# Kernel optimization log

Measured on AMD Instinct MI355X. Metric: run time of the kernel, lower is better.

Reference implementation:

```python
import jax, jax.numpy as jnp
import numpy as np

N, D, H, E, K = 65536, 128, 256, 32, 2


def setup_inputs() -> dict:
    key = jax.random.key(0)
    ks = jax.random.split(key, 7)
    s_in = 1.0 / np.sqrt(D)
    s_hid = 1.0 / np.sqrt(H)
    return {
        "x": jax.random.normal(ks[0], (N, D), dtype=jnp.float32),
        "W1": jax.random.uniform(ks[1], (E, D, H), jnp.float32, -s_in, s_in),
        "b1": jax.random.uniform(ks[2], (E, H), jnp.float32, -s_in, s_in),
        "W2": jax.random.uniform(ks[3], (E, H, D), jnp.float32, -s_hid, s_hid),
        "b2": jax.random.uniform(ks[4], (E, D), jnp.float32, -s_hid, s_hid),
        "Wr": jax.random.uniform(ks[5], (D, E), jnp.float32, -s_in, s_in),
        "br": jax.random.uniform(ks[6], (E,), jnp.float32, -s_in, s_in),
    }


def reference(x, W1, b1, W2, b2, Wr, br):
    # Router (eval mode: no gate noise)
    logits = x @ Wr + br                                  # [N, E]
    scores = jax.nn.softmax(logits, axis=-1)              # [N, E]
    topk_vals, topk_inds = jax.lax.top_k(scores, K)       # [N, K]

    # dispatch_mask: zeros scattered with top-k probs (scatter_ on dim 1)
    n = x.shape[0]
    dispatch_mask = jnp.zeros_like(scores).at[
        jnp.arange(n)[:, None], topk_inds
    ].set(topk_vals)                                      # [N, E]

    # Dense all-experts compute, as in the reference torch.stack
    h = jax.nn.relu(jnp.einsum("nd,edh->neh", x, W1) + b1)   # [N, E, H]
    expert_outputs = jnp.einsum("neh,ehd->ned", h, W2) + b2  # [N, E, D]

    output = jnp.einsum("ned,ne->nd", expert_outputs, dispatch_mask)  # [N, D]

    importance = dispatch_mask.sum(axis=0)                # [E]
    imp_mean = jnp.mean(importance)
    imp_var = jnp.var(importance, ddof=1)                 # torch.var is unbiased
    load_balancing_loss = imp_var / (imp_mean ** 2 + 1e-9)
    return output, load_balancing_loss
```

## Files before the change

kernel.cpp:

```cpp
#include <hip/hip_runtime.h>
#include <hip/hip_bf16.h>
#include <cstdint>
#include <cstddef>

#define N_TOK 65536
#define DIM 128
#define HID 256
#define NE 32
#define TOPK 2

typedef __bf16 bf16x8 __attribute__((ext_vector_type(8)));
typedef float f32x4 __attribute__((ext_vector_type(4)));
typedef unsigned uint4v __attribute__((ext_vector_type(4)));

__device__ __forceinline__ unsigned short f2bf(float f) {
  unsigned u = __builtin_bit_cast(unsigned, f);
  u += 0x7fffu + ((u >> 16) & 1u);
  return (unsigned short)(u >> 16);
}
__device__ __forceinline__ float bf2f(unsigned s) {
  return __builtin_bit_cast(float, s << 16);
}
__device__ __forceinline__ uint2 split2(float f0, float f1) {
  unsigned u0 = __builtin_bit_cast(unsigned, f0);
  unsigned u1 = __builtin_bit_cast(unsigned, f1);
  unsigned hi = (u0 >> 16) | (u1 & 0xffff0000u);
  float r0 = f0 - __builtin_bit_cast(float, u0 & 0xffff0000u);
  float r1 = f1 - __builtin_bit_cast(float, u1 & 0xffff0000u);
  unsigned lo = (__builtin_bit_cast(unsigned, r0) >> 16) |
                (__builtin_bit_cast(unsigned, r1) & 0xffff0000u);
  uint2 ret; ret.x = hi; ret.y = lo;
  return ret;
}

__global__ void k_zero_out(float* __restrict__ out) {
  int t = blockIdx.x * 256 + threadIdx.x;
  float4 z = make_float4(0.f, 0.f, 0.f, 0.f);
  float4* o4 = (float4*)out;
  o4[t] = z;
  o4[t + 1048576] = z;
}

__global__ void k_weights(const float* __restrict__ W1, const float* __restrict__ W2,
                          const float* __restrict__ Wr,
                          unsigned short* __restrict__ w1t, unsigned short* __restrict__ w2t,
                          double* __restrict__ wrt64, unsigned short* __restrict__ wrb,
                          float* __restrict__ ws32, int* __restrict__ n_suspect) {
  int b = blockIdx.x;
  if (b == 512) {
    if (threadIdx.x == 0) *n_suspect = 0;
#pragma unroll
    for (int j = 0; j < 16; ++j) {
      int idx = j * 256 + threadIdx.x;
      int e = idx >> 7, d = idx & 127;
      wrt64[idx] = (double)Wr[d * NE + e];
    }
#pragma unroll
    for (int j = 0; j < 16; ++j) {
      int idx = j * 256 + threadIdx.x;
      int k = idx >> 5, e = idx & 31;
      float w = Wr[k * NE + e];
      unsigned u = __builtin_bit_cast(unsigned, w);
      unsigned short hs = (unsigned short)(u >> 16);
      float r = w - __builtin_bit_cast(float, u & 0xffff0000u);
      unsigned short ls = (unsigned short)(__builtin_bit_cast(unsigned, r) >> 16);
      int nt = e >> 4, n = e & 15, kc = k >> 5, q = (k >> 3) & 3, jj = k & 7;
      size_t base = ((((size_t)nt * 4 + kc) * 4 + q) * 16 + n) * 8 + jj;
      wrb[base] = hs;
      wrb[8192 + base] = ls;
    }
    return;
  }
  if (b == 0 && threadIdx.x < 96) ws32[threadIdx.x] = 0.f;
  const float* in;
  unsigned short* out;
  int K, r0, c0;
  if (b < 256) {
    int e = b >> 3, tt = b & 7;
    in = W1 + (size_t)e * DIM * HID;
    out = w1t + (size_t)e * DIM * HID;
    K = HID;
    r0 = (tt >> 2) * 64; c0 = (tt & 3) * 64;
  } else {
    b -= 256;
    int e = b >> 3, tt = b & 7;
    in = W2 + (size_t)e * HID * DIM;
    out = w2t + (size_t)e * HID * DIM;
    K = DIM;
    r0 = (tt >> 1) * 64; c0 = (tt & 1) * 64;
  }
  __shared__ float tile[64][65];
  int t2 = threadIdx.x;
  int r = t2 >> 2, cs = (t2 & 3) * 16;
  const float* src = in + (size_t)(r0 + r) * K + c0 + cs;
#pragma unroll
  for (int j = 0; j < 4; ++j) {
    float4 v = *(const float4*)(src + j * 4);
    tile[r][cs + j * 4 + 0] = v.x;
    tile[r][cs + j * 4 + 1] = v.y;
    tile[r][cs + j * 4 + 2] = v.z;
    tile[r][cs + j * 4 + 3] = v.w;
  }
  __syncthreads();
#pragma unroll
  for (int p = 0; p < 2; ++p) {
    int orow = p * 32 + (t2 >> 3);
    int oc8 = (t2 & 7) * 8;
    int rr = r0 + oc8;
    unsigned pk[4];
#pragma unroll
    for (int q = 0; q < 4; ++q) {
      unsigned lo = f2bf(tile[oc8 + 2 * q][orow]);
      unsigned hi = f2bf(tile[oc8 + 2 * q + 1][orow]);
      pk[q] = lo | (hi << 16);
    }
    uint4 u;
    u.x = pk[0]; u.y = pk[1]; u.z = pk[2]; u.w = pk[3];
    size_t addr = (size_t)(rr >> 5) * (K * 32) + (size_t)(c0 + orow) * 32 + (rr & 31);
    *(uint4*)(out + addr) = u;
  }
}

__global__ __launch_bounds__(256) void k_router(
    const float* __restrict__ x, const unsigned short* __restrict__ wrb,
    const float* __restrict__ br, int* __restrict__ top_idx, float* __restrict__ top_val,
    int* __restrict__ suspects, int* __restrict__ n_suspect) {
  int t = threadIdx.x;
  int w = t >> 6, l = t & 63, quad = l >> 4, l15 = l & 15;
  int tok0 = blockIdx.x * 256 + w * 64;

  bf16x8 bfr[2][2][4];
#pragma unroll
  for (int s = 0; s < 2; ++s)
#pragma unroll
    for (int nt = 0; nt < 2; ++nt)
#pragma unroll
      for (int kc = 0; kc < 4; ++kc)
        bfr[s][nt][kc] = *(const bf16x8*)(wrb + s * 8192 +
                          ((((size_t)nt * 4 + kc) * 4 + quad) * 16 + l15) * 8);

  f32x4 acc[4][2];
#pragma unroll
  for (int a = 0; a < 4; ++a)
#pragma unroll
    for (int b = 0; b < 2; ++b) {
      f32x4 z = {0.f, 0.f, 0.f, 0.f};
      acc[a][b] = z;
    }

#pragma unroll
  for (int mt = 0; mt < 4; ++mt) {
    const float* xp = x + (size_t)(tok0 + mt * 16 + l15) * DIM + quad * 8;
    float4 va[4][2];
#pragma unroll
    for (int kc = 0; kc < 4; ++kc) {
      const float4* p = (const float4*)(xp + kc * 32);
      va[kc][0] = p[0];
      va[kc][1] = p[1];
    }
#pragma unroll
    for (int kc = 0; kc < 4; ++kc) {
      uint2 s0 = split2(va[kc][0].x, va[kc][0].y);
      uint2 s1 = split2(va[kc][0].z, va[kc][0].w);
      uint2 s2 = split2(va[kc][1].x, va[kc][1].y);
      uint2 s3 = split2(va[kc][1].z, va[kc][1].w);
      uint4v hu, lu;
      hu[0] = s0.x; lu[0] = s0.y;
      hu[1] = s1.x; lu[1] = s1.y;
      hu[2] = s2.x; lu[2] = s2.y;
      hu[3] = s3.x; lu[3] = s3.y;
      bf16x8 ahi = __builtin_bit_cast(bf16x8, hu);
      bf16x8 alo = __builtin_bit_cast(bf16x8, lu);
#pragma unroll
      for (int nt = 0; nt < 2; ++nt) {
        acc[mt][nt] = __builtin_amdgcn_mfma_f32_16x16x32_bf16(ahi, bfr[0][nt][kc], acc[mt][nt], 0, 0, 0);
        acc[mt][nt] = __builtin_amdgcn_mfma_f32_16x16x32_bf16(ahi, bfr[1][nt][kc], acc[mt][nt], 0, 0, 0);
        acc[mt][nt] = __builtin_amdgcn_mfma_f32_16x16x32_bf16(alo, bfr[0][nt][kc], acc[mt][nt], 0, 0, 0);
      }
    }
  }

  float brv0 = br[l15], brv1 = br[16 + l15];
  const float NINF = -3.0e38f;
#pragma unroll
  for (int mt = 0; mt < 4; ++mt) {
#pragma unroll
    for (int r = 0; r < 4; ++r) {
      float c0 = acc[mt][0][r] + brv0;
      float c1 = acc[mt][1][r] + brv1;
      float va = (c0 >= c1) ? c0 : c1;
      int ia = (c0 >= c1) ? l15 : 16 + l15;
#pragma unroll
      for (int off = 1; off < 16; off <<= 1) {
        float ov = __shfl_xor(va, off);
        int oi = __shfl_xor(ia, off);
        if (ov > va || (ov == va && oi < ia)) { va = ov; ia = oi; }
      }
      float v1 = va; int i1 = ia;
      float d0 = (i1 == l15) ? NINF : c0;
      float d1 = (i1 == 16 + l15) ? NINF : c1;
      float vb = (d0 >= d1) ? d0 : d1;
      int ib = (d0 >= d1) ? l15 : 16 + l15;
#pragma unroll
      for (int off = 1; off < 16; off <<= 1) {
        float ov = __shfl_xor(vb, off);
        int oi = __shfl_xor(ib, off);
        if (ov > vb || (ov == vb && oi < ib)) { vb = ov; ib = oi; }
      }
      float v2 = vb; int i2 = ib;
      float e0 = (i1 == l15 || i2 == l15) ? NINF : c0;
      float e1 = (i1 == 16 + l15 || i2 == 16 + l15) ? NINF : c1;
      float vc = (e0 >= e1) ? e0 : e1;
#pragma unroll
      for (int off = 1; off < 16; off <<= 1) {
        float ov = __shfl_xor(vc, off);
        vc = (ov > vc) ? ov : vc;
      }
      float s = __expf(c0 - v1) + __expf(c1 - v1);
#pragma unroll
      for (int off = 1; off < 16; off <<= 1) s += __shfl_xor(s, off);
      if (l15 == 0) {
        int n = tok0 + mt * 16 + quad * 4 + r;
        int2 ti; ti.x = i1; ti.y = i2;
        float2 tv; tv.x = 1.0f / s; tv.y = __expf(v2 - v1) / s;
        ((int2*)top_idx)[n] = ti;
        ((float2*)top_val)[n] = tv;
        if (v2 - vc < 2e-3f) {
          int sidx = atomicAdd(n_suspect, 1);
          suspects[sidx] = n;
        }
      }
    }
  }
}

__global__ __launch_bounds__(256) void k_router_fix(
    const float* __restrict__ x, const double* __restrict__ wrt64,
    const float* __restrict__ br, const int* __restrict__ suspects,
    const int* __restrict__ n_suspect, int* __restrict__ top_idx,
    float* __restrict__ top_val) {
  int t = threadIdx.x;
  int lt = t & 31;
  int gid = blockIdx.x * 8 + (t >> 5);
  int cnt = *n_suspect;
  const double* wcol = wrt64 + lt * DIM;
  for (int s = gid; s < cnt; s += 128 * 8) {
    int n = suspects[s];
    const float* xr = x + (size_t)n * DIM;
    double a = 0.0;
#pragma unroll 8
    for (int d = 0; d < DIM; ++d) a = fma((double)xr[d], wcol[d], a);
    double lv = a + (double)br[lt];

    double v1 = lv; int i1 = lt;
#pragma unroll
    for (int off = 16; off > 0; off >>= 1) {
      double ov = __shfl_xor(v1, off, 32);
      int oi = __shfl_xor(i1, off, 32);
      if (ov > v1 || (ov == v1 && oi < i1)) { v1 = ov; i1 = oi; }
    }
    double lv2 = (lt == i1) ? -1.0e300 : lv;
    double v2 = lv2; int i2 = lt;
#pragma unroll
    for (int off = 16; off > 0; off >>= 1) {
      double ov = __shfl_xor(v2, off, 32);
      int oi = __shfl_xor(i2, off, 32);
      if (ov > v2 || (ov == v2 && oi < i2)) { v2 = ov; i2 = oi; }
    }
    float p = expf((float)(lv - v1));
    float ssum = p;
#pragma unroll
    for (int off = 16; off > 0; off >>= 1) ssum += __shfl_xor(ssum, off, 32);
    if (lt == 0) {
      top_idx[n * 2 + 0] = i1;
      top_idx[n * 2 + 1] = i2;
      top_val[n * 2 + 0] = 1.0f / ssum;
      top_val[n * 2 + 1] = expf((float)(v2 - v1)) / ssum;
    }
  }
}

__global__ __launch_bounds__(256) void k_router_f64(const float* __restrict__ x,
                                                    const double* __restrict__ wrt64,
                                                    const float* __restrict__ br,
                                                    int* __restrict__ top_idx,
                                                    float* __restrict__ top_val) {
  int t = threadIdx.x;
  int lt = t & 31;
  int n = blockIdx.x * 8 + (t >> 5);
  const double* wcol = wrt64 + lt * DIM;
  const float* xr = x + (size_t)n * DIM;
  double a = 0.0;
#pragma unroll 8
  for (int d = 0; d < DIM; ++d) a = fma((double)xr[d], wcol[d], a);
  double lv = a + (double)br[lt];
  double v1 = lv; int i1 = lt;
#pragma unroll
  for (int off = 16; off > 0; off >>= 1) {
    double ov = __shfl_xor(v1, off, 32);
    int oi = __shfl_xor(i1, off, 32);
    if (ov > v1 || (ov == v1 && oi < i1)) { v1 = ov; i1 = oi; }
  }
  double lv2 = (lt == i1) ? -1.0e300 : lv;
  double v2 = lv2; int i2 = lt;
#pragma unroll
  for (int off = 16; off > 0; off >>= 1) {
    double ov = __shfl_xor(v2, off, 32);
    int oi = __shfl_xor(i2, off, 32);
    if (ov > v2 || (ov == v2 && oi < i2)) { v2 = ov; i2 = oi; }
  }
  float p = expf((float)(lv - v1));
  float ssum = p;
#pragma unroll
  for (int off = 16; off > 0; off >>= 1) ssum += __shfl_xor(ssum, off, 32);
  if (lt == 0) {
    top_idx[n * 2 + 0] = i1;
    top_idx[n * 2 + 1] = i2;
    top_val[n * 2 + 0] = 1.0f / ssum;
    top_val[n * 2 + 1] = expf((float)(v2 - v1)) / ssum;
  }
}

__global__ void k_hist(const int* __restrict__ top_idx, const float* __restrict__ top_val,
                       int* __restrict__ counts, float* __restrict__ importance) {
  __shared__ int hc[NE];
  __shared__ float hf[NE];
  int t = threadIdx.x;
  if (t < NE) { hc[t] = 0; hf[t] = 0.f; }
  __syncthreads();
#pragma unroll
  for (int j = 0; j < 2; ++j) {
    int i = (j * 256 + blockIdx.x) * 256 + t;
    int e = top_idx[i];
    atomicAdd(&hc[e], 1);
    atomicAdd(&hf[e], top_val[i]);
  }
  __syncthreads();
  if (t < NE) {
    atomicAdd(&counts[t], hc[t]);
    atomicAdd(&importance[t], hf[t]);
  }
}

__global__ void k_scan_loss(const int* __restrict__ counts, const float* __restrict__ importance,
                            int* __restrict__ offsets, float* __restrict__ out_loss) {
  int t = threadIdx.x;
  if (t < NE) {
    int pc = (counts[t] + 63) & ~63;
    int sc = pc;
#pragma unroll
    for (int off = 1; off < 32; off <<= 1) {
      int ov = __shfl_up(sc, off, 32);
      if (t >= off) sc += ov;
    }
    offsets[t] = sc - pc;
    if (t == NE - 1) offsets[NE] = sc;

    float imp = importance[t];
    float ssum = imp;
#pragma unroll
    for (int off = 16; off > 0; off >>= 1) ssum += __shfl_xor(ssum, off, 32);
    float mean = ssum / 32.0f;
    float dlt = imp - mean;
    float v = dlt * dlt;
#pragma unroll
    for (int off = 16; off > 0; off >>= 1) v += __shfl_xor(v, off, 32);
    float var = v / 31.0f;
    if (t == 0) *out_loss = var / (mean * mean + 1e-9f);
  }
}

__global__ void k_scatter(const int* __restrict__ top_idx, const float* __restrict__ top_val,
                          const int* __restrict__ offsets, int* __restrict__ cursors,
                          int* __restrict__ perm, float* __restrict__ gatev,
                          int* __restrict__ inv) {
  __shared__ int hist[NE], base[NE], cur[NE];
  int t = threadIdx.x;
  if (t < NE) { hist[t] = 0; cur[t] = 0; }
  __syncthreads();
#pragma unroll
  for (int j = 0; j < 4; ++j) {
    int i = blockIdx.x * 1024 + j * 256 + t;
    atomicAdd(&hist[top_idx[i]], 1);
  }
  __syncthreads();
  if (t < NE) base[t] = atomicAdd(&cursors[t], hist[t]);
  __syncthreads();
#pragma unroll
  for (int j = 0; j < 4; ++j) {
    int i = blockIdx.x * 1024 + j * 256 + t;
    int e = top_idx[i];
    int p = atomicAdd(&cur[e], 1);
    int pos = offsets[e] + base[e] + p;
    perm[pos] = i >> 1;
    gatev[pos] = top_val[i];
    inv[i] = pos;
  }
}

template <int YB>
__global__ __launch_bounds__(256, 2) void k_expert(
    const float* __restrict__ x, const unsigned short* __restrict__ w1t,
    const unsigned short* __restrict__ w2t, const float* __restrict__ b1,
    const float* __restrict__ b2, const int* __restrict__ offsets,
    const int* __restrict__ counts, const int* __restrict__ perm,
    const float* __restrict__ gatev, unsigned short* __restrict__ ybuf,
    float* __restrict__ out) {
  __shared__ __align__(16) unsigned char smem[49152];
  unsigned char* xa = smem;
  unsigned char* ha = smem + 16384;

  int slot0 = blockIdx.x * 64;
  if (slot0 >= offsets[NE]) return;
  int e = 0;
#pragma unroll
  for (int i = 1; i < NE; ++i)
    if (slot0 >= offsets[i]) e = i;
  int cnt = counts[e];
  int local0 = slot0 - offsets[e];
  int nvalid = min(64, cnt - local0);

  int t = threadIdx.x;
  int w = t >> 6;
  int l = t & 63;
  int quad = l >> 4;
  int l15 = l & 15;

  const unsigned short* w1e = w1t + (size_t)e * DIM * HID;
  bf16x8 w1f[4][4];
#pragma unroll
  for (int kc = 0; kc < 4; ++kc)
#pragma unroll
    for (int jt = 0; jt < 4; ++jt)
      w1f[kc][jt] = *(const bf16x8*)(w1e + kc * 8192 + (w * 64 + jt * 16 + l15) * 32 + quad * 8);

  {
    int r = t & 63;
    int half = t >> 6;
    unsigned pk[16];
    if (r < nvalid) {
      int token = perm[slot0 + r];
      const float* src = x + (size_t)token * DIM + half * 32;
#pragma unroll
      for (int q = 0; q < 8; ++q) {
        float4 v = ((const float4*)src)[q];
        pk[q * 2 + 0] = (unsigned)f2bf(v.x) | ((unsigned)f2bf(v.y) << 16);
        pk[q * 2 + 1] = (unsigned)f2bf(v.z) | ((unsigned)f2bf(v.w) << 16);
      }
    } else {
#pragma unroll
      for (int q = 0; q < 16; ++q) pk[q] = 0u;
    }
#pragma unroll
    for (int cc = 0; cc < 4; ++cc) {
      uint4 u;
      u.x = pk[cc * 4 + 0]; u.y = pk[cc * 4 + 1]; u.z = pk[cc * 4 + 2]; u.w = pk[cc * 4 + 3];
      *(uint4*)(xa + (half * 4 + cc) * 1024 + r * 16) = u;
    }
  }
  __syncthreads();

  f32x4 acc[4][4];
#pragma unroll
  for (int a = 0; a < 4; ++a)
#pragma unroll
    for (int b = 0; b < 4; ++b) {
      f32x4 z = {0.f, 0.f, 0.f, 0.f};
      acc[a][b] = z;
    }
#pragma unroll
  for (int kc = 0; kc < 4; ++kc) {
    bf16x8 af[4];
#pragma unroll
    for (int rt = 0; rt < 4; ++rt)
      af[rt] = *(const bf16x8*)(xa + (kc * 4 + quad) * 1024 + (rt * 16 + l15) * 16);
#pragma unroll
    for (int rt = 0; rt < 4; ++rt)
#pragma unroll
      for (int jt = 0; jt < 4; ++jt)
        acc[rt][jt] = __builtin_amdgcn_mfma_f32_16x16x32_bf16(af[rt], w1f[kc][jt], acc[rt][jt], 0, 0, 0);
  }

  const unsigned short* w2e = w2t + (size_t)e * HID * DIM;
  bf16x8 w2f[8][2];
#pragma unroll
  for (int hc = 0; hc < 8; ++hc)
#pragma unroll
    for (int jt = 0; jt < 2; ++jt)
      w2f[hc][jt] = *(const bf16x8*)(w2e + hc * 4096 + (w * 32 + jt * 16 + l15) * 32 + quad * 8);

  const float* b1e = b1 + e * HID;
#pragma unroll
  for (int jt = 0; jt < 4; ++jt) {
    int col = w * 64 + jt * 16 + l15;
    float b1v = b1e[col];
    int c = col >> 3;
    int byteoff = (col & 7) * 2;
#pragma unroll
    for (int rt = 0; rt < 4; ++rt) {
#pragma unroll
      for (int r = 0; r < 4; ++r) {
        int tokrow = rt * 16 + quad * 4 + r;
        float v = acc[rt][jt][r] + b1v;
        v = v > 0.f ? v : 0.f;
        *(unsigned short*)(ha + c * 1024 + tokrow * 16 + byteoff) = f2bf(v);
      }
    }
  }
  __syncthreads();

  f32x4 accc[4][2];
#pragma unroll
  for (int a = 0; a < 4; ++a)
#pragma unroll
    for (int b = 0; b < 2; ++b) {
      f32x4 z = {0.f, 0.f, 0.f, 0.f};
      accc[a][b] = z;
    }
#pragma unroll
  for (int hc = 0; hc < 8; ++hc) {
    bf16x8 ah[4];
#pragma unroll
    for (int rt = 0; rt < 4; ++rt)
      ah[rt] = *(const bf16x8*)(ha + (hc * 4 + quad) * 1024 + (rt * 16 + l15) * 16);
#pragma unroll
    for (int rt = 0; rt < 4; ++rt)
#pragma unroll
      for (int jt = 0; jt < 2; ++jt)
        accc[rt][jt] = __builtin_amdgcn_mfma_f32_16x16x32_bf16(ah[rt], w2f[hc][jt], accc[rt][jt], 0, 0, 0);
  }

  int dbase = w * 32;
  float b2v0 = b2[e * DIM + dbase + l15];
  float b2v1 = b2[e * DIM + dbase + 16 + l15];
#pragma unroll
  for (int rt = 0; rt < 4; ++rt) {
#pragma unroll
    for (int r = 0; r < 4; ++r) {
      int tokrow = rt * 16 + quad * 4 + r;
      if (tokrow < nvalid) {
        int pos = slot0 + tokrow;
        float g = gatev[pos];
        if (YB) {
          unsigned short* yrow = ybuf + (size_t)pos * DIM + dbase;
          yrow[l15] = f2bf(g * (accc[rt][0][r] + b2v0));
          yrow[16 + l15] = f2bf(g * (accc[rt][1][r] + b2v1));
        } else {
          int token = perm[pos];
          float* orow = out + (size_t)token * DIM + dbase;
          atomicAdd(&orow[l15], g * (accc[rt][0][r] + b2v0));
          atomicAdd(&orow[16 + l15], g * (accc[rt][1][r] + b2v1));
        }
      }
    }
  }
}

__global__ __launch_bounds__(256) void k_combine(const unsigned short* __restrict__ ybuf,
                                                 const int* __restrict__ inv,
                                                 float* __restrict__ out) {
  int t = threadIdx.x;
  int n = blockIdx.x * 16 + (t >> 4);
  int lane = t & 15;
  int p0 = inv[n * 2 + 0];
  int p1 = inv[n * 2 + 1];
  uint4 a = *((const uint4*)(ybuf + (size_t)p0 * DIM) + lane);
  uint4 b = *((const uint4*)(ybuf + (size_t)p1 * DIM) + lane);
  unsigned av[4] = {a.x, a.y, a.z, a.w}, bv[4] = {b.x, b.y, b.z, b.w};
  float r[8];
#pragma unroll
  for (int q = 0; q < 4; ++q) {
    r[q * 2 + 0] = bf2f(av[q] & 0xffffu) + bf2f(bv[q] & 0xffffu);
    r[q * 2 + 1] = bf2f(av[q] >> 16) + bf2f(bv[q] >> 16);
  }
  float* orow = out + (size_t)n * DIM + lane * 8;
  float4 w0 = {r[0], r[1], r[2], r[3]}, w1 = {r[4], r[5], r[6], r[7]};
  ((float4*)orow)[0] = w0;
  ((float4*)orow)[1] = w1;
}

extern "C" void kernel_launch(void* const* d_in, const int* in_sizes, int n_in,
                              void* d_out, int out_size, void* d_ws, size_t ws_size,
                              hipStream_t stream) {
  const float* x  = (const float*)d_in[0];
  const float* W1 = (const float*)d_in[1];
  const float* b1 = (const float*)d_in[2];
  const float* W2 = (const float*)d_in[3];
  const float* b2 = (const float*)d_in[4];
  const float* Wr = (const float*)d_in[5];
  const float* br = (const float*)d_in[6];
  float* out = (float*)d_out;

  char* ws = (char*)d_ws;
  float* importance   = (float*)(ws + 0);
  int*   counts       = (int*)(ws + 128);
  int*   cursors      = (int*)(ws + 256);
  int*   offsets      = (int*)(ws + 384);
  int*   top_idx      = (int*)(ws + 1024);
  float* top_val      = (float*)(ws + 525312);
  int*   perm         = (int*)(ws + 1049600);
  float* gatev        = (float*)(ws + 1582080);
  int*   inv          = (int*)(ws + 2114560);
  unsigned short* w1t = (unsigned short*)(ws + 2638848);
  unsigned short* w2t = (unsigned short*)(ws + 4736000);
  unsigned short* ybuf = (unsigned short*)(ws + 6833152);
  double* wrt64 = (double*)(ws + 6833152);
  unsigned short* wrb = (unsigned short*)(ws + 6833152 + 32768);
  int* suspects = (int*)(ws + 40911872);
  int* n_suspect = (int*)(ws + 41174016);
  const size_t NEEDED = 41174144;
  bool use_ybuf = ws_size >= NEEDED;

  hipLaunchKernelGGL(k_weights, dim3(513), dim3(256), 0, stream, W1, W2, Wr, w1t, w2t, wrt64,
                     wrb, (float*)ws, n_suspect);
  if (use_ybuf) {
    hipLaunchKernelGGL(k_router, dim3(256), dim3(256), 0, stream, x, wrb, br, top_idx, top_val,
                       suspects, n_suspect);
    hipLaunchKernelGGL(k_router_fix, dim3(128), dim3(256), 0, stream, x, wrt64, br, suspects,
                       n_suspect, top_idx, top_val);
  } else {
    hipLaunchKernelGGL(k_router_f64, dim3(8192), dim3(256), 0, stream, x, wrt64, br, top_idx,
                       top_val);
  }
  hipLaunchKernelGGL(k_hist, dim3(256), dim3(256), 0, stream, top_idx, top_val, counts, importance);
  hipLaunchKernelGGL(k_scan_loss, dim3(1), dim3(64), 0, stream, counts, importance, offsets,
                     out + (size_t)N_TOK * DIM);
  hipLaunchKernelGGL(k_scatter, dim3(128), dim3(256), 0, stream, top_idx, top_val, offsets,
                     cursors, perm, gatev, inv);
  if (use_ybuf) {
    hipLaunchKernelGGL((k_expert<1>), dim3(2080), dim3(256), 0, stream, x, w1t, w2t, b1, b2,
                       offsets, counts, perm, gatev, ybuf, out);
    hipLaunchKernelGGL(k_combine, dim3(4096), dim3(256), 0, stream, ybuf, inv, out);
  } else {
    hipLaunchKernelGGL(k_zero_out, dim3(4096), dim3(256), 0, stream, out);
    hipLaunchKernelGGL((k_expert<0>), dim3(2080), dim3(256), 0, stream, x, w1t, w2t, b1, b2,
                       offsets, counts, perm, gatev, ybuf, out);
  }
}
```

Baseline: 217.4 us.

## Fuse histogram into router, stage bf16 x, merge scan into scatter, remap expert blocks

```diff
diff --git a/kernel.cpp b/kernel.cpp
--- a/kernel.cpp
+++ b/kernel.cpp
@@ -121,13 +121,19 @@
   }
 }
 
-__global__ __launch_bounds__(256) void k_router(
+__global__ __launch_bounds__(256, 2) void k_router(
     const float* __restrict__ x, const unsigned short* __restrict__ wrb,
     const float* __restrict__ br, int* __restrict__ top_idx, float* __restrict__ top_val,
-    int* __restrict__ suspects, int* __restrict__ n_suspect) {
+    unsigned short* __restrict__ xb, int* __restrict__ counts,
+    float* __restrict__ importance, int* __restrict__ suspects,
+    int* __restrict__ n_suspect) {
+  __shared__ int hc[NE];
+  __shared__ float hf[NE];
   int t = threadIdx.x;
+  if (t < NE) { hc[t] = 0; hf[t] = 0.f; }
+  __syncthreads();
   int w = t >> 6, l = t & 63, quad = l >> 4, l15 = l & 15;
-  int tok0 = blockIdx.x * 256 + w * 64;
+  int tok0 = blockIdx.x * 128 + w * 32;
 
   bf16x8 bfr[2][2][4];
 #pragma unroll
@@ -139,9 +145,9 @@
         bfr[s][nt][kc] = *(const bf16x8*)(wrb + s * 8192 +
                           ((((size_t)nt * 4 + kc) * 4 + quad) * 16 + l15) * 8);
 
-  f32x4 acc[4][2];
-#pragma unroll
-  for (int a = 0; a < 4; ++a)
+  f32x4 acc[2][2];
+#pragma unroll
+  for (int a = 0; a < 2; ++a)
 #pragma unroll
     for (int b = 0; b < 2; ++b) {
       f32x4 z = {0.f, 0.f, 0.f, 0.f};
@@ -149,7 +155,7 @@
     }
 
 #pragma unroll
-  for (int mt = 0; mt < 4; ++mt) {
+  for (int mt = 0; mt < 2; ++mt) {
     const float* xp = x + (size_t)(tok0 + mt * 16 + l15) * DIM + quad * 8;
     float4 va[4][2];
 #pragma unroll
@@ -157,6 +163,16 @@
       const float4* p = (const float4*)(xp + kc * 32);
       va[kc][0] = p[0];
       va[kc][1] = p[1];
+    }
+    unsigned short* xrow = xb + (size_t)(tok0 + mt * 16 + l15) * DIM + quad * 8;
+#pragma unroll
+    for (int kc = 0; kc < 4; ++kc) {
+      uint4 u;
+      u.x = (unsigned)f2bf(va[kc][0].x) | ((unsigned)f2bf(va[kc][0].y) << 16);
+      u.y = (unsigned)f2bf(va[kc][0].z) | ((unsigned)f2bf(va[kc][0].w) << 16);
+      u.z = (unsigned)f2bf(va[kc][1].x) | ((unsigned)f2bf(va[kc][1].y) << 16);
+      u.w = (unsigned)f2bf(va[kc][1].z) | ((unsigned)f2bf(va[kc][1].w) << 16);
+      *(uint4*)(xrow + kc * 32) = u;
     }
 #pragma unroll
     for (int kc = 0; kc < 4; ++kc) {
@@ -183,7 +199,7 @@
   float brv0 = br[l15], brv1 = br[16 + l15];
   const float NINF = -3.0e38f;
 #pragma unroll
-  for (int mt = 0; mt < 4; ++mt) {
+  for (int mt = 0; mt < 2; ++mt) {
 #pragma unroll
     for (int r = 0; r < 4; ++r) {
       float c0 = acc[mt][0][r] + brv0;
@@ -225,12 +241,21 @@
         float2 tv; tv.x = 1.0f / s; tv.y = __expf(v2 - v1) / s;
         ((int2*)top_idx)[n] = ti;
         ((float2*)top_val)[n] = tv;
+        atomicAdd(&hc[i1], 1);
+        atomicAdd(&hc[i2], 1);
+        atomicAdd(&hf[i1], tv.x);
+        atomicAdd(&hf[i2], tv.y);
         if (v2 - vc < 2e-3f) {
           int sidx = atomicAdd(n_suspect, 1);
-          suspects[sidx] = n;
+          if (sidx < 65536) suspects[sidx] = n;
         }
       }
     }
+  }
+  __syncthreads();
+  if (t < NE) {
+    atomicAdd(&counts[t], hc[t]);
+    atomicAdd(&importance[t], hf[t]);
   }
 }
 
@@ -238,11 +263,13 @@
     const float* __restrict__ x, const double* __restrict__ wrt64,
     const float* __restrict__ br, const int* __restrict__ suspects,
     const int* __restrict__ n_suspect, int* __restrict__ top_idx,
-    float* __restrict__ top_val) {
+    float* __restrict__ top_val, int* __restrict__ counts,
+    float* __restrict__ importance) {
   int t = threadIdx.x;
   int lt = t & 31;
   int gid = blockIdx.x * 8 + (t >> 5);
   int cnt = *n_suspect;
+  if (cnt > 65536) cnt = 65536;
   const double* wcol = wrt64 + lt * DIM;
   for (int s = gid; s < cnt; s += 128 * 8) {
     int n = suspects[s];
@@ -272,10 +299,22 @@
 #pragma unroll
     for (int off = 16; off > 0; off >>= 1) ssum += __shfl_xor(ssum, off, 32);
     if (lt == 0) {
+      int o1 = top_idx[n * 2 + 0];
+      int o2 = top_idx[n * 2 + 1];
+      float w1v = top_val[n * 2 + 0];
+      float w2v = top_val[n * 2 + 1];
+      float nv1 = 1.0f / ssum;
+      float nv2 = expf((float)(v2 - v1)) / ssum;
+      if (o1 != i1) { atomicAdd(&counts[o1], -1); atomicAdd(&counts[i1], 1); }
+      if (o2 != i2) { atomicAdd(&counts[o2], -1); atomicAdd(&counts[i2], 1); }
+      atomicAdd(&importance[o1], -w1v);
+      atomicAdd(&importance[o2], -w2v);
+      atomicAdd(&importance[i1], nv1);
+      atomicAdd(&importance[i2], nv2);
       top_idx[n * 2 + 0] = i1;
       top_idx[n * 2 + 1] = i2;
-      top_val[n * 2 + 0] = 1.0f / ssum;
-      top_val[n * 2 + 1] = expf((float)(v2 - v1)) / ssum;
+      top_val[n * 2 + 0] = nv1;
+      top_val[n * 2 + 1] = nv2;
     }
   }
 }
@@ -342,10 +381,15 @@
   }
 }
 
-__global__ void k_scan_loss(const int* __restrict__ counts, const float* __restrict__ importance,
-                            int* __restrict__ offsets, float* __restrict__ out_loss) {
+__global__ void k_scatter(const int* __restrict__ top_idx, const float* __restrict__ top_val,
+                          const int* __restrict__ counts, const float* __restrict__ importance,
+                          int* __restrict__ cursors, int* __restrict__ perm,
+                          float* __restrict__ gatev, int* __restrict__ inv,
+                          int* __restrict__ offsets, float* __restrict__ out_loss) {
+  __shared__ int hist[NE], base[NE], cur[NE], soff[NE];
   int t = threadIdx.x;
-  if (t < NE) {
+  if (t < NE) { hist[t] = 0; cur[t] = 0; }
+  if (t < 32) {
     int pc = (counts[t] + 63) & ~63;
     int sc = pc;
 #pragma unroll
@@ -353,30 +397,22 @@
       int ov = __shfl_up(sc, off, 32);
       if (t >= off) sc += ov;
     }
-    offsets[t] = sc - pc;
-    if (t == NE - 1) offsets[NE] = sc;
-
-    float imp = importance[t];
-    float ssum = imp;
-#pragma unroll
-    for (int off = 16; off > 0; off >>= 1) ssum += __shfl_xor(ssum, off, 32);
-    float mean = ssum / 32.0f;
-    float dlt = imp - mean;
-    float v = dlt * dlt;
-#pragma unroll
-    for (int off = 16; off > 0; off >>= 1) v += __shfl_xor(v, off, 32);
-    float var = v / 31.0f;
-    if (t == 0) *out_loss = var / (mean * mean + 1e-9f);
-  }
-}
-
-__global__ void k_scatter(const int* __restrict__ top_idx, const float* __restrict__ top_val,
-                          const int* __restrict__ offsets, int* __restrict__ cursors,
-                          int* __restrict__ perm, float* __restrict__ gatev,
-                          int* __restrict__ inv) {
-  __shared__ int hist[NE], base[NE], cur[NE];
-  int t = threadIdx.x;
-  if (t < NE) { hist[t] = 0; cur[t] = 0; }
+    soff[t] = sc - pc;
+    if (blockIdx.x == 0) {
+      offsets[t] = sc - pc;
+      if (t == 31) offsets[NE] = sc;
+      float imp = importance[t];
+      float ssum = imp;
+#pragma unroll
+      for (int off = 16; off > 0; off >>= 1) ssum += __shfl_xor(ssum, off, 32);
+      float mean = ssum / 32.0f;
+      float dlt = imp - mean;
+      float v = dlt * dlt;
+#pragma unroll
+      for (int off = 16; off > 0; off >>= 1) v += __shfl_xor(v, off, 32);
+      if (t == 0) *out_loss = (v / 31.0f) / (mean * mean + 1e-9f);
+    }
+  }
   __syncthreads();
 #pragma unroll
   for (int j = 0; j < 4; ++j) {
@@ -391,7 +427,7 @@
     int i = blockIdx.x * 1024 + j * 256 + t;
     int e = top_idx[i];
     int p = atomicAdd(&cur[e], 1);
-    int pos = offsets[e] + base[e] + p;
+    int pos = soff[e] + base[e] + p;
     perm[pos] = i >> 1;
     gatev[pos] = top_val[i];
     inv[i] = pos;
@@ -399,18 +435,19 @@
 }
 
 template <int YB>
-__global__ __launch_bounds__(256, 2) void k_expert(
-    const float* __restrict__ x, const unsigned short* __restrict__ w1t,
-    const unsigned short* __restrict__ w2t, const float* __restrict__ b1,
-    const float* __restrict__ b2, const int* __restrict__ offsets,
-    const int* __restrict__ counts, const int* __restrict__ perm,
-    const float* __restrict__ gatev, unsigned short* __restrict__ ybuf,
-    float* __restrict__ out) {
+__global__ __launch_bounds__(256, 3) void k_expert(
+    const float* __restrict__ x, const unsigned short* __restrict__ xb,
+    const unsigned short* __restrict__ w1t, const unsigned short* __restrict__ w2t,
+    const float* __restrict__ b1, const float* __restrict__ b2,
+    const int* __restrict__ offsets, const int* __restrict__ counts,
+    const int* __restrict__ perm, const float* __restrict__ gatev,
+    unsigned short* __restrict__ ybuf, float* __restrict__ out) {
   __shared__ __align__(16) unsigned char smem[49152];
   unsigned char* xa = smem;
   unsigned char* ha = smem + 16384;
 
-  int slot0 = blockIdx.x * 64;
+  int bid = (int)(blockIdx.x & 7) * 260 + (int)(blockIdx.x >> 3);
+  int slot0 = bid * 64;
   if (slot0 >= offsets[NE]) return;
   int e = 0;
 #pragma unroll
@@ -426,15 +463,20 @@
   int quad = l >> 4;
   int l15 = l & 15;
 
-  const unsigned short* w1e = w1t + (size_t)e * DIM * HID;
-  bf16x8 w1f[4][4];
-#pragma unroll
-  for (int kc = 0; kc < 4; ++kc)
-#pragma unroll
-    for (int jt = 0; jt < 4; ++jt)
-      w1f[kc][jt] = *(const bf16x8*)(w1e + kc * 8192 + (w * 64 + jt * 16 + l15) * 32 + quad * 8);
-
-  {
+  if (YB) {
+    uint4 v[4];
+    if (l < nvalid) {
+      const uint4* rowp = (const uint4*)(xb + (size_t)perm[slot0 + l] * DIM);
+#pragma unroll
+      for (int cc = 0; cc < 4; ++cc) v[cc] = rowp[w * 4 + cc];
+    } else {
+#pragma unroll
+      for (int cc = 0; cc < 4; ++cc) { v[cc].x = 0u; v[cc].y = 0u; v[cc].z = 0u; v[cc].w = 0u; }
+    }
+#pragma unroll
+    for (int cc = 0; cc < 4; ++cc)
+      *(uint4*)(xa + (size_t)(w * 4 + cc) * 1024 + l * 16) = v[cc];
+  } else {
     int r = t & 63;
     int half = t >> 6;
     unsigned pk[16];
@@ -443,9 +485,9 @@
       const float* src = x + (size_t)token * DIM + half * 32;
 #pragma unroll
       for (int q = 0; q < 8; ++q) {
-        float4 v = ((const float4*)src)[q];
-        pk[q * 2 + 0] = (unsigned)f2bf(v.x) | ((unsigned)f2bf(v.y) << 16);
-        pk[q * 2 + 1] = (unsigned)f2bf(v.z) | ((unsigned)f2bf(v.w) << 16);
+        float4 vv = ((const float4*)src)[q];
+        pk[q * 2 + 0] = (unsigned)f2bf(vv.x) | ((unsigned)f2bf(vv.y) << 16);
+        pk[q * 2 + 1] = (unsigned)f2bf(vv.z) | ((unsigned)f2bf(vv.w) << 16);
       }
     } else {
 #pragma unroll
@@ -458,6 +500,17 @@
       *(uint4*)(xa + (half * 4 + cc) * 1024 + r * 16) = u;
     }
   }
+
+  const unsigned short* w1e = w1t + (size_t)e * DIM * HID;
+  bf16x8 w1f[4][4];
+#pragma unroll
+  for (int kc = 0; kc < 4; ++kc)
+#pragma unroll
+    for (int jt = 0; jt < 4; ++jt)
+      w1f[kc][jt] = *(const bf16x8*)(w1e + kc * 8192 + (w * 64 + jt * 16 + l15) * 32 + quad * 8);
+
+  float gvl = (l < nvalid) ? gatev[slot0 + l] : 0.f;
+
   __syncthreads();
 
   f32x4 acc[4][4];
@@ -538,9 +591,9 @@
 #pragma unroll
     for (int r = 0; r < 4; ++r) {
       int tokrow = rt * 16 + quad * 4 + r;
+      float g = __shfl(gvl, tokrow);
       if (tokrow < nvalid) {
         int pos = slot0 + tokrow;
-        float g = gatev[pos];
         if (YB) {
           unsigned short* yrow = ybuf + (size_t)pos * DIM + dbase;
           yrow[l15] = f2bf(g * (accc[rt][0][r] + b2v0));
@@ -611,29 +664,32 @@
   const size_t NEEDED = 41174144;
   bool use_ybuf = ws_size >= NEEDED;
 
+  unsigned short* xb = (unsigned short*)out;
+
   hipLaunchKernelGGL(k_weights, dim3(513), dim3(256), 0, stream, W1, W2, Wr, w1t, w2t, wrt64,
                      wrb, (float*)ws, n_suspect);
   if (use_ybuf) {
-    hipLaunchKernelGGL(k_router, dim3(256), dim3(256), 0, stream, x, wrb, br, top_idx, top_val,
-                       suspects, n_suspect);
+    hipLaunchKernelGGL(k_router, dim3(512), dim3(256), 0, stream, x, wrb, br, top_idx, top_val,
+                       xb, counts, importance, suspects, n_suspect);
     hipLaunchKernelGGL(k_router_fix, dim3(128), dim3(256), 0, stream, x, wrt64, br, suspects,
-                       n_suspect, top_idx, top_val);
+                       n_suspect, top_idx, top_val, counts, importance);
+    hipLaunchKernelGGL(k_scatter, dim3(128), dim3(256), 0, stream, top_idx, top_val, counts,
+                       importance, cursors, perm, gatev, inv, offsets,
+                       out + (size_t)N_TOK * DIM);
+    hipLaunchKernelGGL((k_expert<1>), dim3(2080), dim3(256), 0, stream, x, xb, w1t, w2t, b1, b2,
+                       offsets, counts, perm, gatev, ybuf, out);
+    hipLaunchKernelGGL(k_combine, dim3(4096), dim3(256), 0, stream, ybuf, inv, out);
   } else {
     hipLaunchKernelGGL(k_router_f64, dim3(8192), dim3(256), 0, stream, x, wrt64, br, top_idx,
                        top_val);
-  }
-  hipLaunchKernelGGL(k_hist, dim3(256), dim3(256), 0, stream, top_idx, top_val, counts, importance);
-  hipLaunchKernelGGL(k_scan_loss, dim3(1), dim3(64), 0, stream, counts, importance, offsets,
-                     out + (size_t)N_TOK * DIM);
-  hipLaunchKernelGGL(k_scatter, dim3(128), dim3(256), 0, stream, top_idx, top_val, offsets,
-                     cursors, perm, gatev, inv);
-  if (use_ybuf) {
-    hipLaunchKernelGGL((k_expert<1>), dim3(2080), dim3(256), 0, stream, x, w1t, w2t, b1, b2,
-                       offsets, counts, perm, gatev, ybuf, out);
-    hipLaunchKernelGGL(k_combine, dim3(4096), dim3(256), 0, stream, ybuf, inv, out);
-  } else {
+    hipLaunchKernelGGL(k_hist, dim3(256), dim3(256), 0, stream, top_idx, top_val, counts,
+                       importance);
+    hipLaunchKernelGGL(k_scatter, dim3(128), dim3(256), 0, stream, top_idx, top_val, counts,
+                       importance, cursors, perm, gatev, inv, offsets,
+                       out + (size_t)N_TOK * DIM);
     hipLaunchKernelGGL(k_zero_out, dim3(4096), dim3(256), 0, stream, out);
-    hipLaunchKernelGGL((k_expert<0>), dim3(2080), dim3(256), 0, stream, x, w1t, w2t, b1, b2,
-                       offsets, counts, perm, gatev, ybuf, out);
-  }
-}
+    hipLaunchKernelGGL((k_expert<0>), dim3(2080), dim3(256), 0, stream, x,
+                       (const unsigned short*)0, w1t, w2t, b1, b2, offsets, counts, perm, gatev,
+                       ybuf, out);
+  }
+}
```

Measured after the change: 208.7 us. 1.04x faster.
